# Optimization experiments

Measured on AMD Instinct MI355X. Metric: run time of the kernel, lower is better.

## Reference

```python
import jax, jax.numpy as jnp
import numpy as np

N, E, F, H, C = 100000, 3200000, 128, 256, 47
EPS = 1e-5


def setup_inputs() -> dict:
    key = jax.random.key(0)
    ks = jax.random.split(key, 12)
    x = jax.random.normal(ks[0], (N, F), dtype=jnp.float32)
    edge_index = jax.random.randint(ks[1], (2, E), 0, N, dtype=jnp.int64)
    relations = jax.random.randint(ks[2], (E,), 0, 4, dtype=jnp.int64)
    def lin(k, fan_in, fan_out):
        return jax.random.normal(k, (fan_in, fan_out), dtype=jnp.float32) / np.sqrt(fan_in)
    W0 = lin(ks[3], F, H); b0 = jnp.zeros((H,), jnp.float32)
    W1 = lin(ks[4], H, H); b1 = jnp.zeros((H,), jnp.float32)
    W2 = lin(ks[5], H, C); b2 = jnp.zeros((C,), jnp.float32)
    g0 = jnp.ones((H,), jnp.float32); be0 = jnp.zeros((H,), jnp.float32)
    g1 = jnp.ones((H,), jnp.float32); be1 = jnp.zeros((H,), jnp.float32)
    return {"x": x, "edge_index": edge_index, "relations": relations,
            "W0": W0, "b0": b0, "g0": g0, "be0": be0,
            "W1": W1, "b1": b1, "g1": g1, "be1": be1,
            "W2": W2, "b2": b2}


def _gcn_conv(x, W, b, src, dst, n_nodes):
    # GCNConv: linear transform, add self-loops, symmetric degree normalization,
    # gather-scale-scatter aggregation, bias add.
    h = x @ W  # [N, out]
    self_loop = jnp.arange(n_nodes, dtype=src.dtype)
    s = jnp.concatenate([src, self_loop])
    d = jnp.concatenate([dst, self_loop])
    deg = jax.ops.segment_sum(jnp.ones(d.shape[0], h.dtype), d, num_segments=n_nodes)
    dinv = jnp.where(deg > 0, jax.lax.rsqrt(deg), 0.0)
    coef = dinv[s] * dinv[d]  # [E+N]
    out = jax.ops.segment_sum(h[s] * coef[:, None], d, num_segments=n_nodes)
    return out + b


def _batch_norm(x, gamma, beta):
    mean = jnp.mean(x, axis=0)
    var = jnp.var(x, axis=0)
    return (x - mean) * jax.lax.rsqrt(var + EPS) * gamma + beta


def reference(x, edge_index, relations, W0, b0, g0, be0, W1, b1, g1, be1, W2, b2):
    src, dst = edge_index[0], edge_index[1]
    n = x.shape[0]
    h = _gcn_conv(x, W0, b0, src, dst, n)
    h = jax.nn.relu(_batch_norm(h, g0, be0))  # dropout is identity in eval
    h = _gcn_conv(h, W1, b1, src, dst, n)
    h = jax.nn.relu(_batch_norm(h, g1, be1))
    h = _gcn_conv(h, W2, b2, src, dst, n)
    return jax.nn.log_softmax(h, axis=-1)
```

## Files before the change

### kernel.cpp

```cpp
#include <hip/hip_runtime.h>
#include <hip/hip_fp8.h>
#include <math.h>

#define NN 100000
#define NE 3200000
#define FIN 128
#define HD 256
#define CO 47
#define COP 48
#define NBKT 196
#define G 1024
#define CHUNK 3125

typedef _Float16 h2 __attribute__((ext_vector_type(2)));
typedef _Float16 h4 __attribute__((ext_vector_type(4)));
typedef _Float16 h8 __attribute__((ext_vector_type(8)));
typedef float f32x2 __attribute__((ext_vector_type(2)));
typedef float f32x4 __attribute__((ext_vector_type(4)));
typedef unsigned int u32x4 __attribute__((ext_vector_type(4)));


__global__ __launch_bounds__(256) void hist_kernel(const int* __restrict__ dst,
                                                   int* __restrict__ hist) {
    __shared__ int h[NBKT];
    int tid = threadIdx.x;
    for (int i = tid; i < NBKT; i += 256) h[i] = 0;
    __syncthreads();
    int base = blockIdx.x * CHUNK;
    for (int i = tid; i < CHUNK; i += 256)
        atomicAdd(&h[dst[base + i] >> 9], 1);
    __syncthreads();
    for (int i = tid; i < NBKT; i += 256) hist[i * G + blockIdx.x] = h[i];
}

__global__ __launch_bounds__(256) void rowscan_kernel(int* __restrict__ hist,
                                                      int* __restrict__ btot) {
    __shared__ int sums[256];
    int b = blockIdx.x, t = threadIdx.x;
    int base = b * G + t * 4;
    int4 v = *(int4*)&hist[base];
    int i0 = v.x, i1 = i0 + v.y, i2 = i1 + v.z, i3 = i2 + v.w;
    sums[t] = i3;
    __syncthreads();
    #pragma unroll
    for (int off = 1; off < 256; off <<= 1) {
        int u = (t >= off) ? sums[t - off] : 0;
        __syncthreads();
        sums[t] += u;
        __syncthreads();
    }
    int excl = sums[t] - i3;
    hist[base] = excl;
    hist[base + 1] = excl + i0;
    hist[base + 2] = excl + i1;
    hist[base + 3] = excl + i2;
    if (t == 255) btot[b] = sums[255];
}

__global__ void totscan_kernel(const int* __restrict__ btot, int* __restrict__ bbase) {
    __shared__ int tmp[256];
    int t = threadIdx.x;
    int v = (t < NBKT) ? btot[t] : 0;
    tmp[t] = v;
    __syncthreads();
    #pragma unroll
    for (int off = 1; off < 256; off <<= 1) {
        int u = (t >= off) ? tmp[t - off] : 0;
        __syncthreads();
        tmp[t] += u;
        __syncthreads();
    }
    if (t < NBKT) bbase[t] = tmp[t] - v;
    if (t == NBKT - 1) bbase[NBKT] = tmp[t];
}

__global__ __launch_bounds__(256) void scatter_kernel(const int* __restrict__ src,
                                                      const int* __restrict__ dst,
                                                      const int* __restrict__ hscan,
                                                      const int* __restrict__ bbase,
                                                      int* __restrict__ epk) {
    __shared__ int cur[NBKT];
    int tid = threadIdx.x;
    for (int i = tid; i < NBKT; i += 256)
        cur[i] = hscan[i * G + blockIdx.x] + bbase[i];
    __syncthreads();
    int base = blockIdx.x * CHUNK;
    for (int i = tid; i < CHUNK; i += 256) {
        int e = base + i;
        int d = dst[e];
        int slot = atomicAdd(&cur[d >> 9], 1);
        epk[slot] = ((d & 511) << 17) | src[e];
    }
}

__global__ __launch_bounds__(256) void bucket_fill_kernel(
    const int* __restrict__ bbase, const int* __restrict__ epk,
    int* __restrict__ csr, int* __restrict__ offs, float* __restrict__ dinv)
{
    __shared__ int deg[512], cur[512], a0[512], a1[512];
    int tid = threadIdx.x, b = blockIdx.x;
    int ebeg = bbase[b], eend = bbase[b + 1];
    deg[tid] = 0; deg[tid + 256] = 0;
    __syncthreads();
    for (int e = ebeg + tid; e < eend; e += 256)
        atomicAdd(&deg[((unsigned)epk[e]) >> 17], 1);
    __syncthreads();
    a0[tid] = deg[tid]; a0[tid + 256] = deg[tid + 256];
    __syncthreads();
    int* pin = a0; int* pout = a1;
    for (int off = 1; off < 512; off <<= 1) {
        #pragma unroll
        for (int q = 0; q < 2; ++q) {
            int p = tid + q * 256;
            pout[p] = pin[p] + ((p >= off) ? pin[p - off] : 0);
        }
        __syncthreads();
        int* t = pin; pin = pout; pout = t;
    }
    #pragma unroll
    for (int q = 0; q < 2; ++q) {
        int i = tid + q * 256;
        int excl = pin[i] - deg[i];
        cur[i] = excl;
        int node = b * 512 + i;
        if (node < NN) {
            offs[node] = ebeg + excl;
            dinv[node] = rsqrtf((float)deg[i] + 1.0f);
        }
    }
    if (b == 0 && tid == 0) offs[NN] = NE;
    __syncthreads();
    for (int e = ebeg + tid; e < eend; e += 256) {
        int pk = epk[e];
        int p = atomicAdd(&cur[((unsigned)pk) >> 17], 1);
        csr[ebeg + p] = pk & 0x1FFFF;
    }
}


template<int K>
__global__ void wtrans_kernel(const float* __restrict__ W, _Float16* __restrict__ Wt,
                              int N, int NP) {
    int i = blockIdx.x * 256 + threadIdx.x;
    if (i >= NP * K) return;
    int n = i / K, k = i % K;
    float v = (n < N) ? W[(size_t)k * N + n] : 0.0f;
    Wt[i] = (_Float16)v;
}


__global__ void conv_x_kernel(const float* __restrict__ x, const float* __restrict__ dinv,
                              unsigned* __restrict__ xq) {
    int i = blockIdx.x * 256 + threadIdx.x;
    if (i >= NN * FIN / 4) return;
    int r = i >> 5;
    float4 v = ((const float4*)x)[i];
    float dv = dinv[r];
    int u = __builtin_amdgcn_cvt_pk_fp8_f32(v.x * dv, v.y * dv, 0, false);
    u = __builtin_amdgcn_cvt_pk_fp8_f32(v.z * dv, v.w * dv, u, true);
    xq[i] = (unsigned)u;
}


__global__ __launch_bounds__(256) void agg128_kernel(
    const unsigned short* __restrict__ xq, const int* __restrict__ offs,
    const int* __restrict__ csr, const float* __restrict__ dinv,
    _Float16* __restrict__ out)
{
    int lane = threadIdx.x & 63;
    int v = blockIdx.x * 4 + (threadIdx.x >> 6);
    unsigned sv = xq[(size_t)v * 64 + lane];
    f32x2 acc = __builtin_amdgcn_cvt_pk_f32_fp8((int)sv, false);
    int b = offs[v], e = offs[v + 1], j = b;
    int s[8];
    if (j + 8 <= e) {
        #pragma unroll
        for (int q = 0; q < 8; ++q) s[q] = csr[j + q];
    }
    for (; j + 8 <= e; ) {
        int nj = j + 8;
        int ns[8];
        if (nj + 8 <= e) {
            #pragma unroll
            for (int q = 0; q < 8; ++q) ns[q] = csr[nj + q];
        }
        #pragma unroll
        for (int q = 0; q < 8; ++q) {
            unsigned t = xq[(size_t)s[q] * 64 + lane];
            acc += __builtin_amdgcn_cvt_pk_f32_fp8((int)t, false);
        }
        #pragma unroll
        for (int q = 0; q < 8; ++q) s[q] = ns[q];
        j = nj;
    }
    for (; j < e; ++j) {
        unsigned t = xq[(size_t)csr[j] * 64 + lane];
        acc += __builtin_amdgcn_cvt_pk_f32_fp8((int)t, false);
    }
    float dv = dinv[v];
    h2 o; o[0] = (_Float16)(acc[0] * dv); o[1] = (_Float16)(acc[1] * dv);
    ((h2*)out)[(size_t)v * 64 + lane] = o;
}

__global__ __launch_bounds__(256) void agg256_kernel(
    const unsigned* __restrict__ t1q, const int* __restrict__ offs,
    const int* __restrict__ csr, const float* __restrict__ dinv,
    _Float16* __restrict__ out)
{
    int lane = threadIdx.x & 63;
    int v = blockIdx.x * 4 + (threadIdx.x >> 6);
    unsigned sv = t1q[(size_t)v * 64 + lane];
    f32x2 acc01 = __builtin_amdgcn_cvt_pk_f32_fp8((int)sv, false);
    f32x2 acc23 = __builtin_amdgcn_cvt_pk_f32_fp8((int)sv, true);
    int b = offs[v], e = offs[v + 1], j = b;
    int s[8];
    if (j + 8 <= e) {
        #pragma unroll
        for (int q = 0; q < 8; ++q) s[q] = csr[j + q];
    }
    for (; j + 8 <= e; ) {
        int nj = j + 8;
        int ns[8];
        if (nj + 8 <= e) {
            #pragma unroll
            for (int q = 0; q < 8; ++q) ns[q] = csr[nj + q];
        }
        #pragma unroll
        for (int q = 0; q < 8; ++q) {
            unsigned t = t1q[(size_t)s[q] * 64 + lane];
            acc01 += __builtin_amdgcn_cvt_pk_f32_fp8((int)t, false);
            acc23 += __builtin_amdgcn_cvt_pk_f32_fp8((int)t, true);
        }
        #pragma unroll
        for (int q = 0; q < 8; ++q) s[q] = ns[q];
        j = nj;
    }
    for (; j < e; ++j) {
        unsigned t = t1q[(size_t)csr[j] * 64 + lane];
        acc01 += __builtin_amdgcn_cvt_pk_f32_fp8((int)t, false);
        acc23 += __builtin_amdgcn_cvt_pk_f32_fp8((int)t, true);
    }
    float dv = dinv[v];
    h4 o; o[0] = (_Float16)(acc01[0] * dv); o[1] = (_Float16)(acc01[1] * dv);
    o[2] = (_Float16)(acc23[0] * dv); o[3] = (_Float16)(acc23[1] * dv);
    ((h4*)out)[(size_t)v * 64 + lane] = o;
}

__global__ __launch_bounds__(256) void agg47_lsm_kernel(
    const _Float16* __restrict__ t2, const int* __restrict__ offs,
    const int* __restrict__ csr, const float* __restrict__ dinv,
    const float* __restrict__ bias, float* __restrict__ out)
{
    int lane = threadIdx.x & 63;
    int v = blockIdx.x * 4 + (threadIdx.x >> 6);
    bool act = lane < CO;
    float acc = act ? (float)t2[(size_t)v * COP + lane] : 0.0f;
    int b = offs[v], e = offs[v + 1], j = b;
    int s[8];
    if (j + 8 <= e) {
        #pragma unroll
        for (int q = 0; q < 8; ++q) s[q] = csr[j + q];
    }
    for (; j + 8 <= e; ) {
        int nj = j + 8;
        int ns[8];
        if (nj + 8 <= e) {
            #pragma unroll
            for (int q = 0; q < 8; ++q) ns[q] = csr[nj + q];
        }
        if (act) {
            #pragma unroll
            for (int q = 0; q < 8; ++q) acc += (float)t2[(size_t)s[q] * COP + lane];
        }
        #pragma unroll
        for (int q = 0; q < 8; ++q) s[q] = ns[q];
        j = nj;
    }
    for (; j < e; ++j) if (act) acc += (float)t2[(size_t)csr[j] * COP + lane];
    float val = act ? fmaf(acc, dinv[v], bias[lane]) : -1e30f;
    float m = val;
    #pragma unroll
    for (int o = 32; o > 0; o >>= 1) m = fmaxf(m, __shfl_xor(m, o, 64));
    float ex = act ? expf(val - m) : 0.0f;
    float sum = ex;
    #pragma unroll
    for (int o = 32; o > 0; o >>= 1) sum += __shfl_xor(sum, o, 64);
    if (act) out[(size_t)v * CO + lane] = val - m - logf(sum);
}


#define LDS_PAD 8

template<int K, bool XFORM, bool EPI_DINV, bool OUT8>
__global__ __launch_bounds__(256) void mfma_gemm_big(
    const _Float16* __restrict__ A, int lda,
    const _Float16* __restrict__ Wt,
    const float* __restrict__ ss, const float* __restrict__ dinv,
    void* __restrict__ outp, int ldo)
{
    __shared__ __align__(16) _Float16 As[128][64 + LDS_PAD];
    __shared__ __align__(16) _Float16 Bs[128][64 + LDS_PAD];
    __shared__ float SS[2 * K];
    const int row0 = (blockIdx.x >> 1) * 128;
    const int col0 = (blockIdx.x & 1) * 128;
    const int tid = threadIdx.x;
    if (XFORM) {
        for (int i = tid; i < 2 * K; i += 256) SS[i] = ss[i];
    }
    const int lane = tid & 63;
    const int wv = tid >> 6;
    const int wr = wv >> 1, wc = wv & 1;
    const int fr = lane & 15;
    const int kb = (lane >> 4) * 8;

    f32x4 acc[4][4];
    #pragma unroll
    for (int m = 0; m < 4; ++m)
        #pragma unroll
        for (int n = 0; n < 4; ++n)
            acc[m][n] = (f32x4){0.f, 0.f, 0.f, 0.f};

    if (XFORM) __syncthreads();

    for (int k0 = 0; k0 < K; k0 += 64) {
        #pragma unroll
        for (int p = 0; p < 4; ++p) {
            int c = p * 256 + tid;
            int m = c >> 3, kk = (c & 7) * 8;
            int r = row0 + m;
            h8 av = {};
            if (r < NN) av = *(const h8*)&A[(size_t)r * lda + k0 + kk];
            if (XFORM) {
                #pragma unroll
                for (int j = 0; j < 8; ++j) {
                    float a = (float)av[j];
                    a = fmaxf(fmaf(a, SS[k0 + kk + j], SS[K + k0 + kk + j]), 0.0f);
                    av[j] = (_Float16)a;
                }
            }
            *(h8*)&As[m][kk] = av;
        }
        #pragma unroll
        for (int p = 0; p < 4; ++p) {
            int c = p * 256 + tid;
            int n = c >> 3, kk = (c & 7) * 8;
            h8 bv = *(const h8*)&Wt[(size_t)(col0 + n) * K + k0 + kk];
            *(h8*)&Bs[n][kk] = bv;
        }
        __syncthreads();
        #pragma unroll
        for (int ks = 0; ks < 2; ++ks) {
            h8 a[4], b[4];
            #pragma unroll
            for (int m = 0; m < 4; ++m)
                a[m] = *(const h8*)&As[wr * 64 + m * 16 + fr][ks * 32 + kb];
            #pragma unroll
            for (int n = 0; n < 4; ++n)
                b[n] = *(const h8*)&Bs[wc * 64 + n * 16 + fr][ks * 32 + kb];
            #pragma unroll
            for (int m = 0; m < 4; ++m)
                #pragma unroll
                for (int n = 0; n < 4; ++n)
                    acc[m][n] = __builtin_amdgcn_mfma_f32_16x16x32_f16(a[m], b[n], acc[m][n], 0, 0, 0);
        }
        __syncthreads();
    }

    const int fq = lane >> 4;
    if (OUT8) {
        unsigned char* stg = (unsigned char*)&As[0][0];
        #pragma unroll
        for (int m = 0; m < 4; ++m) {
            #pragma unroll
            for (int j = 0; j < 4; ++j) {
                int rr = wr * 64 + m * 16 + fq * 4 + j;
                int r = row0 + rr;
                float dv = (EPI_DINV && r < NN) ? dinv[r] : 1.0f;
                #pragma unroll
                for (int n = 0; n < 4; n += 2) {
                    int cc0 = wc * 64 + n * 16 + fr;
                    float v0 = acc[m][n][j] * dv;
                    float v1 = acc[m][n + 1][j] * dv;
                    int pk = __builtin_amdgcn_cvt_pk_fp8_f32(v0, v1, 0, false);
                    stg[rr * 128 + cc0] = (unsigned char)(pk & 0xFF);
                    stg[rr * 128 + cc0 + 16] = (unsigned char)((pk >> 8) & 0xFF);
                }
            }
        }
        __syncthreads();
        #pragma unroll
        for (int p = 0; p < 4; ++p) {
            int rr = p * 32 + (tid >> 3);
            int cc = (tid & 7) * 16;
            int r = row0 + rr;
            if (r < NN)
                *(u32x4*)&((unsigned char*)outp)[(size_t)r * ldo + col0 + cc] =
                    *(u32x4*)&stg[rr * 128 + cc];
        }
    } else {
        #pragma unroll
        for (int m = 0; m < 4; ++m) {
            #pragma unroll
            for (int j = 0; j < 4; ++j) {
                int r = row0 + wr * 64 + m * 16 + fq * 4 + j;
                if (r >= NN) continue;
                float dv = EPI_DINV ? dinv[r] : 1.0f;
                #pragma unroll
                for (int n = 0; n < 4; ++n) {
                    int c = col0 + wc * 64 + n * 16 + fr;
                    ((_Float16*)outp)[(size_t)r * ldo + c] = (_Float16)(acc[m][n][j] * dv);
                }
            }
        }
    }
}


template<int K, bool XFORM, bool EPI_DINV>
__global__ __launch_bounds__(256) void mfma_gemm_kernel(
    const _Float16* __restrict__ A, int lda,
    const _Float16* __restrict__ Wt,
    const float* __restrict__ ss, const float* __restrict__ dinv,
    _Float16* __restrict__ out, int ldo, int ncolsO)
{
    __shared__ __align__(16) _Float16 As[128][32 + LDS_PAD];
    __shared__ __align__(16) _Float16 Bs[64][32 + LDS_PAD];
    __shared__ float SS[2 * K];
    const int row0 = blockIdx.x * 128;
    const int col0 = blockIdx.y * 64;
    const int tid = threadIdx.x;
    if (XFORM) {
        for (int i = tid; i < 2 * K; i += 256) SS[i] = ss[i];
    }
    const int lane = tid & 63;
    const int wv = tid >> 6;
    const int wr = wv >> 1, wc = wv & 1;
    const int fr = lane & 15;
    const int kb = (lane >> 4) * 8;

    f32x4 acc[4][2];
    #pragma unroll
    for (int m = 0; m < 4; ++m)
        #pragma unroll
        for (int n = 0; n < 2; ++n)
            acc[m][n] = (f32x4){0.f, 0.f, 0.f, 0.f};

    if (XFORM) __syncthreads();

    for (int k0 = 0; k0 < K; k0 += 32) {
        #pragma unroll
        for (int p = 0; p < 2; ++p) {
            int idx = (p * 256 + tid) * 8;
            int m = idx >> 5, kk = idx & 31;
            int r = row0 + m;
            h8 av = {};
            if (r < NN) av = *(const h8*)&A[(size_t)r * lda + k0 + kk];
            if (XFORM) {
                #pragma unroll
                for (int j = 0; j < 8; ++j) {
                    float a = (float)av[j];
                    a = fmaxf(fmaf(a, SS[k0 + kk + j], SS[K + k0 + kk + j]), 0.0f);
                    av[j] = (_Float16)a;
                }
            }
            *(h8*)&As[m][kk] = av;
        }
        {
            int idx = tid * 8;
            int n = idx >> 5, kk = idx & 31;
            h8 bv = *(const h8*)&Wt[(size_t)(col0 + n) * K + k0 + kk];
            *(h8*)&Bs[n][kk] = bv;
        }
        __syncthreads();
        h8 a[4], b[2];
        #pragma unroll
        for (int m = 0; m < 4; ++m)
            a[m] = *(const h8*)&As[wr * 64 + m * 16 + fr][kb];
        #pragma unroll
        for (int n = 0; n < 2; ++n)
            b[n] = *(const h8*)&Bs[wc * 32 + n * 16 + fr][kb];
        #pragma unroll
        for (int m = 0; m < 4; ++m)
            #pragma unroll
            for (int n = 0; n < 2; ++n)
                acc[m][n] = __builtin_amdgcn_mfma_f32_16x16x32_f16(a[m], b[n], acc[m][n], 0, 0, 0);
        __syncthreads();
    }

    const int fq = lane >> 4;
    #pragma unroll
    for (int m = 0; m < 4; ++m) {
        #pragma unroll
        for (int j = 0; j < 4; ++j) {
            int r = row0 + wr * 64 + m * 16 + fq * 4 + j;
            if (r >= NN) continue;
            float dv = EPI_DINV ? dinv[r] : 1.0f;
            #pragma unroll
            for (int n = 0; n < 2; ++n) {
                int c = col0 + wc * 32 + n * 16 + fr;
                if (c < ncolsO) out[(size_t)r * ldo + c] = (_Float16)(acc[m][n][j] * dv);
            }
        }
    }
}


__global__ __launch_bounds__(256) void bn_part_kernel(const _Float16* __restrict__ h,
                                                      float* __restrict__ part) {
    int tid = threadIdx.x;
    int fg = tid & 63;
    int rg = tid >> 6;
    float s1[4] = {}, s2[4] = {};
    for (int r = blockIdx.x * 4 + rg; r < NN; r += 4096) {
        h4 v = ((const h4*)(h + (size_t)r * HD))[fg];
        #pragma unroll
        for (int j = 0; j < 4; ++j) {
            float f = (float)v[j];
            s1[j] += f; s2[j] += f * f;
        }
    }
    __shared__ float sm[256][8];
    #pragma unroll
    for (int j = 0; j < 4; ++j) { sm[tid][j] = s1[j]; sm[tid][4 + j] = s2[j]; }
    __syncthreads();
    if (tid < 64) {
        float o1[4] = {}, o2[4] = {};
        #pragma unroll
        for (int r = 0; r < 4; ++r)
            #pragma unroll
            for (int j = 0; j < 4; ++j) {
                o1[j] += sm[r * 64 + tid][j];
                o2[j] += sm[r * 64 + tid][4 + j];
            }
        #pragma unroll
        for (int j = 0; j < 4; ++j) {
            part[(size_t)blockIdx.x * 512 + tid * 4 + j] = o1[j];
            part[(size_t)blockIdx.x * 512 + 256 + tid * 4 + j] = o2[j];
        }
    }
}

__global__ __launch_bounds__(256) void bn_reduce_kernel(const float* __restrict__ part,
                                                        const float* __restrict__ g,
                                                        const float* __restrict__ be,
                                                        float* __restrict__ ss) {
    int f = blockIdx.x * 32 + (threadIdx.x & 31);
    int c = threadIdx.x >> 5;
    float s1 = 0.f, s2 = 0.f;
    for (int b = c; b < 1024; b += 8) {
        s1 += part[(size_t)b * 512 + f];
        s2 += part[(size_t)b * 512 + 256 + f];
    }
    __shared__ float m1[8][32], m2[8][32];
    m1[c][threadIdx.x & 31] = s1; m2[c][threadIdx.x & 31] = s2;
    __syncthreads();
    if (threadIdx.x < 32) {
        float t1 = 0.f, t2 = 0.f;
        #pragma unroll
        for (int q = 0; q < 8; ++q) { t1 += m1[q][threadIdx.x]; t2 += m2[q][threadIdx.x]; }
        float mean = t1 * (1.0f / NN);
        float var = t2 * (1.0f / NN) - mean * mean;
        float sc = g[f] * rsqrtf(var + 1e-5f);
        ss[f] = sc;
        ss[HD + f] = be[f] - mean * sc;
    }
}


extern "C" void kernel_launch(void* const* d_in, const int* in_sizes, int n_in,
                              void* d_out, int out_size, void* d_ws, size_t ws_size,
                              hipStream_t stream) {
    const float* x   = (const float*)d_in[0];
    const int*   ei  = (const int*)d_in[1];
    const float* W0  = (const float*)d_in[3];
    const float* g0  = (const float*)d_in[5];
    const float* be0 = (const float*)d_in[6];
    const float* W1  = (const float*)d_in[7];
    const float* g1  = (const float*)d_in[9];
    const float* be1 = (const float*)d_in[10];
    const float* W2  = (const float*)d_in[11];
    const float* b2  = (const float*)d_in[12];
    float* out = (float*)d_out;

    const int* src = ei;
    const int* dst = ei + NE;

    const size_t S = 51200000;
    char* ws = (char*)d_ws;
    unsigned*  xq  = (unsigned*)ws;
    unsigned*  t1q = (unsigned*)ws;
    _Float16*  t2  = (_Float16*)ws;
    _Float16*  a0  = (_Float16*)(ws + 25600000);
    _Float16*  S2  = (_Float16*)(ws + S);
    char* base2 = ws + 2 * S;
    int*   csr  = (int*)  (base2);
    int*   offs = (int*)  (base2 + 12800000);
    float* dinv = (float*)(base2 + 13200064);
    float* ssb  = (float*)(base2 + 13602112);
    int*   btot = (int*)  (base2 + 13604160);
    int*   bbase= (int*)  (base2 + 13605184);
    _Float16* wt0 = (_Float16*)(base2 + 13608320);
    _Float16* wt1 = (_Float16*)(base2 + 13673856);
    _Float16* wt2 = (_Float16*)(base2 + 13804928);
    int*   hist = (int*)  (base2 + 13837696);
    int*   epk  = (int*)  (base2 + 14640576);
    float* part = (float*)(base2 + 27440576);

    hist_kernel<<<G, 256, 0, stream>>>(dst, hist);
    rowscan_kernel<<<NBKT, 256, 0, stream>>>(hist, btot);
    totscan_kernel<<<1, 256, 0, stream>>>(btot, bbase);
    scatter_kernel<<<G, 256, 0, stream>>>(src, dst, hist, bbase, epk);
    bucket_fill_kernel<<<NBKT, 256, 0, stream>>>(bbase, epk, csr, offs, dinv);

    wtrans_kernel<FIN><<<(256 * FIN + 255) / 256, 256, 0, stream>>>(W0, wt0, HD, HD);
    wtrans_kernel<HD><<<(256 * HD + 255) / 256, 256, 0, stream>>>(W1, wt1, HD, HD);
    wtrans_kernel<HD><<<(64 * HD + 255) / 256, 256, 0, stream>>>(W2, wt2, CO, 64);

    const int MB = (NN + 127) / 128;

    conv_x_kernel<<<(NN * FIN / 4 + 255) / 256, 256, 0, stream>>>(x, dinv, xq);
    agg128_kernel<<<NN / 4, 256, 0, stream>>>((const unsigned short*)xq, offs, csr, dinv, a0);
    mfma_gemm_big<FIN, false, false, false><<<MB * 2, 256, 0, stream>>>(
        a0, FIN, wt0, nullptr, dinv, S2, HD);

    bn_part_kernel<<<1024, 256, 0, stream>>>(S2, part);
    bn_reduce_kernel<<<8, 256, 0, stream>>>(part, g0, be0, ssb);

    mfma_gemm_big<HD, true, true, true><<<MB * 2, 256, 0, stream>>>(
        S2, HD, wt1, ssb, dinv, t1q, HD);
    agg256_kernel<<<NN / 4, 256, 0, stream>>>(t1q, offs, csr, dinv, S2);

    bn_part_kernel<<<1024, 256, 0, stream>>>(S2, part);
    bn_reduce_kernel<<<8, 256, 0, stream>>>(part, g1, be1, ssb);

    mfma_gemm_kernel<HD, true, true><<<dim3(MB, 1), 256, 0, stream>>>(
        S2, HD, wt2, ssb, dinv, t2, COP, CO);
    agg47_lsm_kernel<<<NN / 4, 256, 0, stream>>>(t2, offs, csr, dinv, b2, out);
}
```

Baseline: 583.8 us.

## Store layer-2 activations and logits in fp8, fuse layer-0 BN stats into GEMM

The layer-2 aggregation now writes fp8 instead of fp16. The final small GEMM reads that fp8 input and writes fp8 logits padded to 64 columns, and the last aggregation kernel gathers 4 classes per lane from 16-byte rows, which cuts gather traffic for the memory-bound edge aggregations. The first big GEMM also accumulates BatchNorm sum and sum-of-squares through LDS and global atomics, replacing a separate stats pass over its output. This adds fp8 quantisation error on activations and logits, uses single-pass variance, and adds atomic contention.

```diff
diff --git a/kernel.cpp b/kernel.cpp
--- a/kernel.cpp
+++ b/kernel.cpp
@@ -7,7 +7,6 @@
 #define FIN 128
 #define HD 256
 #define CO 47
-#define COP 48
 #define NBKT 196
 #define G 1024
 #define CHUNK 3125
@@ -17,6 +16,7 @@
 typedef _Float16 h8 __attribute__((ext_vector_type(8)));
 typedef float f32x2 __attribute__((ext_vector_type(2)));
 typedef float f32x4 __attribute__((ext_vector_type(4)));
+typedef unsigned int u32x2 __attribute__((ext_vector_type(2)));
 typedef unsigned int u32x4 __attribute__((ext_vector_type(4)));
 
 
@@ -205,7 +205,7 @@
 __global__ __launch_bounds__(256) void agg256_kernel(
     const unsigned* __restrict__ t1q, const int* __restrict__ offs,
     const int* __restrict__ csr, const float* __restrict__ dinv,
-    _Float16* __restrict__ out)
+    unsigned* __restrict__ out)
 {
     int lane = threadIdx.x & 63;
     int v = blockIdx.x * 4 + (threadIdx.x >> 6);
@@ -241,20 +241,25 @@
         acc23 += __builtin_amdgcn_cvt_pk_f32_fp8((int)t, true);
     }
     float dv = dinv[v];
-    h4 o; o[0] = (_Float16)(acc01[0] * dv); o[1] = (_Float16)(acc01[1] * dv);
-    o[2] = (_Float16)(acc23[0] * dv); o[3] = (_Float16)(acc23[1] * dv);
-    ((h4*)out)[(size_t)v * 64 + lane] = o;
+    int pk = __builtin_amdgcn_cvt_pk_fp8_f32(acc01[0] * dv, acc01[1] * dv, 0, false);
+    pk = __builtin_amdgcn_cvt_pk_fp8_f32(acc23[0] * dv, acc23[1] * dv, pk, true);
+    out[(size_t)v * 64 + lane] = (unsigned)pk;
 }
 
 __global__ __launch_bounds__(256) void agg47_lsm_kernel(
-    const _Float16* __restrict__ t2, const int* __restrict__ offs,
+    const unsigned* __restrict__ t2q, const int* __restrict__ offs,
     const int* __restrict__ csr, const float* __restrict__ dinv,
     const float* __restrict__ bias, float* __restrict__ out)
 {
     int lane = threadIdx.x & 63;
     int v = blockIdx.x * 4 + (threadIdx.x >> 6);
-    bool act = lane < CO;
-    float acc = act ? (float)t2[(size_t)v * COP + lane] : 0.0f;
+    bool act = lane < 16;
+    f32x2 a01 = {0.f, 0.f}, a23 = {0.f, 0.f};
+    if (act) {
+        unsigned u = t2q[(size_t)v * 16 + lane];
+        a01 = __builtin_amdgcn_cvt_pk_f32_fp8((int)u, false);
+        a23 = __builtin_amdgcn_cvt_pk_f32_fp8((int)u, true);
+    }
     int b = offs[v], e = offs[v + 1], j = b;
     int s[8];
     if (j + 8 <= e) {
@@ -270,43 +275,70 @@
         }
         if (act) {
             #pragma unroll
-            for (int q = 0; q < 8; ++q) acc += (float)t2[(size_t)s[q] * COP + lane];
+            for (int q = 0; q < 8; ++q) {
+                unsigned t = t2q[(size_t)s[q] * 16 + lane];
+                a01 += __builtin_amdgcn_cvt_pk_f32_fp8((int)t, false);
+                a23 += __builtin_amdgcn_cvt_pk_f32_fp8((int)t, true);
+            }
         }
         #pragma unroll
         for (int q = 0; q < 8; ++q) s[q] = ns[q];
         j = nj;
     }
-    for (; j < e; ++j) if (act) acc += (float)t2[(size_t)csr[j] * COP + lane];
-    float val = act ? fmaf(acc, dinv[v], bias[lane]) : -1e30f;
-    float m = val;
-    #pragma unroll
-    for (int o = 32; o > 0; o >>= 1) m = fmaxf(m, __shfl_xor(m, o, 64));
-    float ex = act ? expf(val - m) : 0.0f;
-    float sum = ex;
-    #pragma unroll
-    for (int o = 32; o > 0; o >>= 1) sum += __shfl_xor(sum, o, 64);
-    if (act) out[(size_t)v * CO + lane] = val - m - logf(sum);
+    for (; j < e; ++j) {
+        if (act) {
+            unsigned t = t2q[(size_t)csr[j] * 16 + lane];
+            a01 += __builtin_amdgcn_cvt_pk_f32_fp8((int)t, false);
+            a23 += __builtin_amdgcn_cvt_pk_f32_fp8((int)t, true);
+        }
+    }
+    float dv = dinv[v];
+    float vals[4] = {a01[0], a01[1], a23[0], a23[1]};
+    float vv[4];
+    #pragma unroll
+    for (int k = 0; k < 4; ++k) {
+        int c = 4 * lane + k;
+        vv[k] = (act && c < CO) ? fmaf(vals[k], dv, bias[c]) : -1e30f;
+    }
+    float m = fmaxf(fmaxf(vv[0], vv[1]), fmaxf(vv[2], vv[3]));
+    #pragma unroll
+    for (int o = 8; o > 0; o >>= 1) m = fmaxf(m, __shfl_xor(m, o, 64));
+    float sum = 0.f;
+    #pragma unroll
+    for (int k = 0; k < 4; ++k) sum += (vv[k] > -1e29f) ? expf(vv[k] - m) : 0.f;
+    #pragma unroll
+    for (int o = 8; o > 0; o >>= 1) sum += __shfl_xor(sum, o, 64);
+    float lse = m + logf(sum);
+    if (act) {
+        #pragma unroll
+        for (int k = 0; k < 4; ++k) {
+            int c = 4 * lane + k;
+            if (c < CO) out[(size_t)v * CO + c] = vv[k] - lse;
+        }
+    }
 }
 
 
 #define LDS_PAD 8
 
-template<int K, bool XFORM, bool EPI_DINV, bool OUT8>
+template<int K, bool XFORM, bool EPI_DINV, bool OUT8, bool BNSTAT>
 __global__ __launch_bounds__(256) void mfma_gemm_big(
     const _Float16* __restrict__ A, int lda,
     const _Float16* __restrict__ Wt,
     const float* __restrict__ ss, const float* __restrict__ dinv,
-    void* __restrict__ outp, int ldo)
+    void* __restrict__ outp, int ldo, float* __restrict__ part8)
 {
     __shared__ __align__(16) _Float16 As[128][64 + LDS_PAD];
     __shared__ __align__(16) _Float16 Bs[128][64 + LDS_PAD];
     __shared__ float SS[2 * K];
+    __shared__ float cstat[256];
     const int row0 = (blockIdx.x >> 1) * 128;
     const int col0 = (blockIdx.x & 1) * 128;
     const int tid = threadIdx.x;
     if (XFORM) {
         for (int i = tid; i < 2 * K; i += 256) SS[i] = ss[i];
     }
+    if (BNSTAT) cstat[tid] = 0.f;
     const int lane = tid & 63;
     const int wv = tid >> 6;
     const int wr = wv >> 1, wc = wv & 1;
@@ -320,7 +352,7 @@
         for (int n = 0; n < 4; ++n)
             acc[m][n] = (f32x4){0.f, 0.f, 0.f, 0.f};
 
-    if (XFORM) __syncthreads();
+    if (XFORM || BNSTAT) __syncthreads();
 
     for (int k0 = 0; k0 < K; k0 += 64) {
         #pragma unroll
@@ -398,6 +430,7 @@
                     *(u32x4*)&stg[rr * 128 + cc];
         }
     } else {
+        float ps[4] = {}, pq[4] = {};
         #pragma unroll
         for (int m = 0; m < 4; ++m) {
             #pragma unroll
@@ -408,30 +441,42 @@
                 #pragma unroll
                 for (int n = 0; n < 4; ++n) {
                     int c = col0 + wc * 64 + n * 16 + fr;
-                    ((_Float16*)outp)[(size_t)r * ldo + c] = (_Float16)(acc[m][n][j] * dv);
+                    float val = acc[m][n][j] * dv;
+                    ((_Float16*)outp)[(size_t)r * ldo + c] = (_Float16)val;
+                    if (BNSTAT) { ps[n] += val; pq[n] += val * val; }
                 }
             }
         }
-    }
-}
-
-
-template<int K, bool XFORM, bool EPI_DINV>
-__global__ __launch_bounds__(256) void mfma_gemm_kernel(
-    const _Float16* __restrict__ A, int lda,
+        if (BNSTAT) {
+            #pragma unroll
+            for (int n = 0; n < 4; ++n) {
+                int cc = wc * 64 + n * 16 + fr;
+                atomicAdd(&cstat[cc], ps[n]);
+                atomicAdd(&cstat[128 + cc], pq[n]);
+            }
+            __syncthreads();
+            if (tid < 128) {
+                int rep = (blockIdx.x & 7) * 512;
+                atomicAdd(&part8[rep + col0 + tid], cstat[tid]);
+                atomicAdd(&part8[rep + 256 + col0 + tid], cstat[128 + tid]);
+            }
+        }
+    }
+}
+
+
+__global__ __launch_bounds__(256) void mfma_gemm2_kernel(
+    const unsigned* __restrict__ Aq,
     const _Float16* __restrict__ Wt,
     const float* __restrict__ ss, const float* __restrict__ dinv,
-    _Float16* __restrict__ out, int ldo, int ncolsO)
+    unsigned char* __restrict__ t2q)
 {
     __shared__ __align__(16) _Float16 As[128][32 + LDS_PAD];
     __shared__ __align__(16) _Float16 Bs[64][32 + LDS_PAD];
-    __shared__ float SS[2 * K];
+    __shared__ float SS[2 * HD];
     const int row0 = blockIdx.x * 128;
-    const int col0 = blockIdx.y * 64;
     const int tid = threadIdx.x;
-    if (XFORM) {
-        for (int i = tid; i < 2 * K; i += 256) SS[i] = ss[i];
-    }
+    for (int i = tid; i < 2 * HD; i += 256) SS[i] = ss[i];
     const int lane = tid & 63;
     const int wv = tid >> 6;
     const int wr = wv >> 1, wc = wv & 1;
@@ -445,30 +490,36 @@
         for (int n = 0; n < 2; ++n)
             acc[m][n] = (f32x4){0.f, 0.f, 0.f, 0.f};
 
-    if (XFORM) __syncthreads();
-
-    for (int k0 = 0; k0 < K; k0 += 32) {
+    __syncthreads();
+
+    for (int k0 = 0; k0 < HD; k0 += 32) {
         #pragma unroll
         for (int p = 0; p < 2; ++p) {
             int idx = (p * 256 + tid) * 8;
             int m = idx >> 5, kk = idx & 31;
             int r = row0 + m;
-            h8 av = {};
-            if (r < NN) av = *(const h8*)&A[(size_t)r * lda + k0 + kk];
-            if (XFORM) {
-                #pragma unroll
-                for (int j = 0; j < 8; ++j) {
-                    float a = (float)av[j];
-                    a = fmaxf(fmaf(a, SS[k0 + kk + j], SS[K + k0 + kk + j]), 0.0f);
-                    av[j] = (_Float16)a;
-                }
+            float vals[8] = {};
+            if (r < NN) {
+                u32x2 u = *(const u32x2*)&Aq[(size_t)r * 64 + ((k0 + kk) >> 2)];
+                f32x2 p0 = __builtin_amdgcn_cvt_pk_f32_fp8((int)u[0], false);
+                f32x2 p1 = __builtin_amdgcn_cvt_pk_f32_fp8((int)u[0], true);
+                f32x2 p2 = __builtin_amdgcn_cvt_pk_f32_fp8((int)u[1], false);
+                f32x2 p3 = __builtin_amdgcn_cvt_pk_f32_fp8((int)u[1], true);
+                vals[0] = p0[0]; vals[1] = p0[1]; vals[2] = p1[0]; vals[3] = p1[1];
+                vals[4] = p2[0]; vals[5] = p2[1]; vals[6] = p3[0]; vals[7] = p3[1];
+            }
+            h8 av;
+            #pragma unroll
+            for (int j = 0; j < 8; ++j) {
+                float a = fmaxf(fmaf(vals[j], SS[k0 + kk + j], SS[HD + k0 + kk + j]), 0.0f);
+                av[j] = (_Float16)a;
             }
             *(h8*)&As[m][kk] = av;
         }
         {
             int idx = tid * 8;
             int n = idx >> 5, kk = idx & 31;
-            h8 bv = *(const h8*)&Wt[(size_t)(col0 + n) * K + k0 + kk];
+            h8 bv = *(const h8*)&Wt[(size_t)n * HD + k0 + kk];
             *(h8*)&Bs[n][kk] = bv;
         }
         __syncthreads();
@@ -488,36 +539,68 @@
     }
 
     const int fq = lane >> 4;
+    unsigned char* stg = (unsigned char*)&As[0][0];
     #pragma unroll
     for (int m = 0; m < 4; ++m) {
         #pragma unroll
         for (int j = 0; j < 4; ++j) {
-            int r = row0 + wr * 64 + m * 16 + fq * 4 + j;
-            if (r >= NN) continue;
-            float dv = EPI_DINV ? dinv[r] : 1.0f;
-            #pragma unroll
-            for (int n = 0; n < 2; ++n) {
-                int c = col0 + wc * 32 + n * 16 + fr;
-                if (c < ncolsO) out[(size_t)r * ldo + c] = (_Float16)(acc[m][n][j] * dv);
-            }
-        }
-    }
-}
-
-
-__global__ __launch_bounds__(256) void bn_part_kernel(const _Float16* __restrict__ h,
-                                                      float* __restrict__ part) {
+            int rr = wr * 64 + m * 16 + fq * 4 + j;
+            int r = row0 + rr;
+            float dv = (r < NN) ? dinv[r] : 1.0f;
+            int cc0 = wc * 32 + fr;
+            float v0 = acc[m][0][j] * dv;
+            float v1 = acc[m][1][j] * dv;
+            int pk = __builtin_amdgcn_cvt_pk_fp8_f32(v0, v1, 0, false);
+            stg[rr * 64 + cc0] = (unsigned char)(pk & 0xFF);
+            stg[rr * 64 + cc0 + 16] = (unsigned char)((pk >> 8) & 0xFF);
+        }
+    }
+    __syncthreads();
+    #pragma unroll
+    for (int p = 0; p < 2; ++p) {
+        int idx = p * 256 + tid;
+        int rr = idx >> 2;
+        int cc = (idx & 3) * 16;
+        int r = row0 + rr;
+        if (r < NN)
+            *(u32x4*)&t2q[(size_t)r * 64 + cc] = *(u32x4*)&stg[rr * 64 + cc];
+    }
+}
+
+
+__global__ void bn_finalize8_kernel(const float* __restrict__ part8,
+                                    const float* __restrict__ g,
+                                    const float* __restrict__ be,
+                                    float* __restrict__ ss) {
+    int t = threadIdx.x;
+    float s1 = 0.f, s2 = 0.f;
+    #pragma unroll
+    for (int x = 0; x < 8; ++x) {
+        s1 += part8[x * 512 + t];
+        s2 += part8[x * 512 + 256 + t];
+    }
+    float mean = s1 * (1.0f / NN);
+    float var = s2 * (1.0f / NN) - mean * mean;
+    float sc = g[t] * rsqrtf(var + 1e-5f);
+    ss[t] = sc;
+    ss[HD + t] = be[t] - mean * sc;
+}
+
+__global__ __launch_bounds__(256) void bn_part8_kernel(const unsigned* __restrict__ h,
+                                                       float* __restrict__ part) {
     int tid = threadIdx.x;
     int fg = tid & 63;
     int rg = tid >> 6;
     float s1[4] = {}, s2[4] = {};
     for (int r = blockIdx.x * 4 + rg; r < NN; r += 4096) {
-        h4 v = ((const h4*)(h + (size_t)r * HD))[fg];
-        #pragma unroll
-        for (int j = 0; j < 4; ++j) {
-            float f = (float)v[j];
-            s1[j] += f; s2[j] += f * f;
-        }
+        unsigned u = h[(size_t)r * 64 + fg];
+        f32x2 a = __builtin_amdgcn_cvt_pk_f32_fp8((int)u, false);
+        f32x2 b = __builtin_amdgcn_cvt_pk_f32_fp8((int)u, true);
+        float f0 = a[0], f1 = a[1], f2 = b[0], f3 = b[1];
+        s1[0] += f0; s2[0] += f0 * f0;
+        s1[1] += f1; s2[1] += f1 * f1;
+        s1[2] += f2; s2[2] += f2 * f2;
+        s1[3] += f3; s2[3] += f3 * f3;
     }
     __shared__ float sm[256][8];
     #pragma unroll
@@ -587,11 +670,12 @@
 
     const size_t S = 51200000;
     char* ws = (char*)d_ws;
-    unsigned*  xq  = (unsigned*)ws;
-    unsigned*  t1q = (unsigned*)ws;
-    _Float16*  t2  = (_Float16*)ws;
-    _Float16*  a0  = (_Float16*)(ws + 25600000);
-    _Float16*  S2  = (_Float16*)(ws + S);
+    unsigned*       xq  = (unsigned*)ws;
+    unsigned*       t1q = (unsigned*)ws;
+    unsigned char*  t2q = (unsigned char*)ws;
+    _Float16*       a0  = (_Float16*)(ws + 25600000);
+    _Float16*       S2  = (_Float16*)(ws + S);
+    unsigned*       h1q = (unsigned*)(ws + S);
     char* base2 = ws + 2 * S;
     int*   csr  = (int*)  (base2);
     int*   offs = (int*)  (base2 + 12800000);
@@ -605,6 +689,7 @@
     int*   hist = (int*)  (base2 + 13837696);
     int*   epk  = (int*)  (base2 + 14640576);
     float* part = (float*)(base2 + 27440576);
+    float* part8= (float*)(base2 + 29537728);
 
     hist_kernel<<<G, 256, 0, stream>>>(dst, hist);
     rowscan_kernel<<<NBKT, 256, 0, stream>>>(hist, btot);
@@ -618,22 +703,20 @@
 
     const int MB = (NN + 127) / 128;
 
+    hipMemsetAsync(part8, 0, 8 * 512 * sizeof(float), stream);
     conv_x_kernel<<<(NN * FIN / 4 + 255) / 256, 256, 0, stream>>>(x, dinv, xq);
     agg128_kernel<<<NN / 4, 256, 0, stream>>>((const unsigned short*)xq, offs, csr, dinv, a0);
-    mfma_gemm_big<FIN, false, false, false><<<MB * 2, 256, 0, stream>>>(
-        a0, FIN, wt0, nullptr, dinv, S2, HD);
-
-    bn_part_kernel<<<1024, 256, 0, stream>>>(S2, part);
-    bn_reduce_kernel<<<8, 256, 0, stream>>>(part, g0, be0, ssb);
-
-    mfma_gemm_big<HD, true, true, true><<<MB * 2, 256, 0, stream>>>(
-        S2, HD, wt1, ssb, dinv, t1q, HD);
-    agg256_kernel<<<NN / 4, 256, 0, stream>>>(t1q, offs, csr, dinv, S2);
-
-    bn_part_kernel<<<1024, 256, 0, stream>>>(S2, part);
+    mfma_gemm_big<FIN, false, false, false, true><<<MB * 2, 256, 0, stream>>>(
+        a0, FIN, wt0, nullptr, dinv, S2, HD, part8);
+    bn_finalize8_kernel<<<1, HD, 0, stream>>>(part8, g0, be0, ssb);
+
+    mfma_gemm_big<HD, true, true, true, false><<<MB * 2, 256, 0, stream>>>(
+        S2, HD, wt1, ssb, dinv, t1q, HD, nullptr);
+    agg256_kernel<<<NN / 4, 256, 0, stream>>>(t1q, offs, csr, dinv, h1q);
+
+    bn_part8_kernel<<<1024, 256, 0, stream>>>(h1q, part);
     bn_reduce_kernel<<<8, 256, 0, stream>>>(part, g1, be1, ssb);
 
-    mfma_gemm_kernel<HD, true, true><<<dim3(MB, 1), 256, 0, stream>>>(
-        S2, HD, wt2, ssb, dinv, t2, COP, CO);
-    agg47_lsm_kernel<<<NN / 4, 256, 0, stream>>>(t2, offs, csr, dinv, b2, out);
-}
+    mfma_gemm2_kernel<<<MB, 256, 0, stream>>>(h1q, wt2, ssb, dinv, t2q);
+    agg47_lsm_kernel<<<NN / 4, 256, 0, stream>>>((const unsigned*)t2q, offs, csr, dinv, b2, out);
+}
```

After: 554.8 us. 1.05x faster.
